# Kernel optimization log

Hardware: AMD Instinct MI355X
Metric: run time of the kernel (lower is better)

Reference implementation:

```python
import jax, jax.numpy as jnp
import numpy as np

C_RGLRU = 8.0

def _rg_lru(x, wa, ba, wx, bx, lam):
    # x: [B, L, D]. Griffin RG-LRU (De et al. 2024).
    r = jax.nn.sigmoid(jnp.einsum('bld,ed->ble', x, wa) + ba)
    i = jax.nn.sigmoid(jnp.einsum('bld,ed->ble', x, wx) + bx)
    log_a = -C_RGLRU * r * jax.nn.softplus(lam)          # [B,L,D], <= 0
    a = jnp.exp(log_a)
    mult = jnp.sqrt(jnp.maximum(1.0 - jnp.exp(2.0 * log_a), 0.0))
    b = mult * (i * x)
    def combine(c1, c2):
        a1, b1 = c1
        a2, b2 = c2
        return a1 * a2, a2 * b1 + b2
    _, h = jax.lax.associative_scan(combine, (a, b), axis=1)
    return h

def setup_inputs() -> dict:
    key = jax.random.key(0)
    ks = jax.random.split(key, 12)
    B, L, D, R = 4, 2048, 2048, 2560
    s_d = 1.0 / np.sqrt(D)
    s_r = 1.0 / np.sqrt(R)
    s_c = 1.0 / np.sqrt(R * 4)
    return {
        'x':      jax.random.normal(ks[0], (B, L, D), jnp.float32),
        'w1':     jax.random.normal(ks[1], (R, D), jnp.float32) * s_d,
        'b1':     jnp.zeros((R,), jnp.float32),
        'conv_w': jax.random.normal(ks[2], (R, R, 4), jnp.float32) * s_c,
        'conv_b': jnp.zeros((R,), jnp.float32),
        'wa':     jax.random.normal(ks[3], (R, R), jnp.float32) * s_r,
        'ba':     jnp.zeros((R,), jnp.float32),
        'wx':     jax.random.normal(ks[4], (R, R), jnp.float32) * s_r,
        'bx':     jnp.zeros((R,), jnp.float32),
        'lam':    jax.random.uniform(ks[5], (R,), jnp.float32, 0.5, 2.0),
        'w2':     jax.random.normal(ks[6], (D, R), jnp.float32) * s_r,
        'b2':     jnp.zeros((D,), jnp.float32),
    }

def reference(x, w1, b1, conv_w, conv_b, wa, ba, wx, bx, lam, w2, b2):
    # linear1 + SiLU: [B,L,D] -> [B,L,R]
    h = jax.nn.silu(jnp.einsum('bld,rd->blr', x, w1) + b1)
    # temporal conv1d: kernel 4, dilation 2, padding 3 both sides (as in torch)
    hc = h.transpose(0, 2, 1)  # [B,R,L]
    hc = jax.lax.conv_general_dilated(
        hc, conv_w, window_strides=(1,), padding=[(3, 3)],
        rhs_dilation=(2,), dimension_numbers=('NCH', 'OIH', 'NCH'))
    hc = hc + conv_b[None, :, None]
    h = hc.transpose(0, 2, 1)  # [B,L,R]
    # RG-LRU gated linear recurrence
    h = _rg_lru(h, wa, ba, wx, bx, lam)
    # linear2: [B,L,R] -> [B,L,D]
    return jnp.einsum('blr,dr->bld', h, w2) + b2
```

## Files before the change

### kernel.cpp

```cpp
#include <hip/hip_runtime.h>

#define B_  4
#define L_  2048
#define D_  2048
#define R_  2560
#define BL_ (B_ * L_)

#define CHK_  16
#define CLEN_ (L_ / CHK_)

typedef unsigned short u16;
typedef unsigned int   u32;

typedef __attribute__((ext_vector_type(8))) short short8;
typedef __attribute__((ext_vector_type(4))) float f32x4;
typedef __attribute__((ext_vector_type(4))) int   int4v;

static __device__ __forceinline__ u16 f2bf(float f) {
  u32 x = __float_as_uint(f);
  x += 0x7fffu + ((x >> 16) & 1u);
  return (u16)(x >> 16);
}
static __device__ __forceinline__ float bf2f(u16 u) {
  return __uint_as_float(((u32)u) << 16);
}

static __device__ __forceinline__ void gld16(const u16* g, u16* l) {
  __builtin_amdgcn_global_load_lds(
      (const __attribute__((address_space(1))) void*)g,
      (__attribute__((address_space(3))) void*)l, 16, 0, 0);
}

__global__ void cvt_bf16(const float* __restrict__ src, u16* __restrict__ dst, int n) {
  int i = blockIdx.x * blockDim.x + threadIdx.x;
  int stride = gridDim.x * blockDim.x;
  for (; i < n; i += stride) dst[i] = f2bf(src[i]);
}

__global__ void cvt_convw(const float* __restrict__ cw, u16* __restrict__ out) {
  int i = blockIdx.x * blockDim.x + threadIdx.x;
  if (i >= R_ * R_) return;
  const float4 v = *(const float4*)(cw + (size_t)i * 4);
  out[(size_t)0 * R_ * R_ + i] = f2bf(v.x);
  out[(size_t)1 * R_ * R_ + i] = f2bf(v.y);
  out[(size_t)2 * R_ * R_ + i] = f2bf(v.z);
  out[(size_t)3 * R_ * R_ + i] = f2bf(v.w);
}

template <int ACT , int OBF16 >
__global__ __launch_bounds__(256)
void gemm_bt(const u16* __restrict__ A, const u16* __restrict__ Bm,
             const float* __restrict__ bias, void* __restrict__ Cv,
             int M, int N, int K) {
  __shared__ u16 As[128 * 32];
  __shared__ u16 Bs[128 * 32];
  const int tid  = threadIdx.x;
  const int bm   = blockIdx.x * 128, bn = blockIdx.y * 128;
  const int wave = tid >> 6, lane = tid & 63;
  const int wm   = (wave >> 1) * 64, wn = (wave & 1) * 64;
  const int q    = lane >> 4, r16 = lane & 15;
  const int lrow = lane >> 2;
  const int gch  = (lane & 3) ^ (lrow & 3);

  f32x4 acc[4][4] = {};

  const int swz = (q ^ (r16 & 3)) * 8;

  for (int kk = 0; kk < K; kk += 32) {
#pragma unroll
    for (int p = 0; p < 2; ++p) {
      const int rb = wave * 32 + p * 16;
      gld16(A  + (size_t)(bm + rb + lrow) * K + kk + gch * 8, &As[rb * 32]);
      gld16(Bm + (size_t)(bn + rb + lrow) * K + kk + gch * 8, &Bs[rb * 32]);
    }
    __syncthreads();
    short8 af[4], bfr[4];
#pragma unroll
    for (int i = 0; i < 4; ++i)
      af[i] = *(const short8*)(&As[(wm + i * 16 + r16) * 32 + swz]);
#pragma unroll
    for (int j = 0; j < 4; ++j)
      bfr[j] = *(const short8*)(&Bs[(wn + j * 16 + r16) * 32 + swz]);
#pragma unroll
    for (int i = 0; i < 4; ++i)
#pragma unroll
      for (int j = 0; j < 4; ++j)
        acc[i][j] = __builtin_amdgcn_mfma_f32_16x16x32_bf16(af[i], bfr[j], acc[i][j], 0, 0, 0);
    __syncthreads();
  }

#pragma unroll
  for (int i = 0; i < 4; ++i) {
    const int row = bm + wm + i * 16 + q * 4;
#pragma unroll
    for (int j = 0; j < 4; ++j) {
      const int col = bn + wn + j * 16 + r16;
      const float bv = bias[col];
#pragma unroll
      for (int rr = 0; rr < 4; ++rr) {
        float v = acc[i][j][rr] + bv;
        if (ACT == 1) v = v / (1.f + __expf(-v));
        const size_t off = (size_t)(row + rr) * N + col;
        if (OBF16) ((u16*)Cv)[off] = f2bf(v);
        else       ((float*)Cv)[off] = v;
      }
    }
  }
}

__global__ __launch_bounds__(256)
void conv_gemm(const u16* __restrict__ A, const u16* __restrict__ CW,
               const float* __restrict__ bias, u16* __restrict__ C) {
  __shared__ u16 As[128 * 32];
  __shared__ u16 Bs[128 * 32];
  const int tid  = threadIdx.x;
  const int bm   = blockIdx.x * 128, bn = blockIdx.y * 128;
  const int wave = tid >> 6, lane = tid & 63;
  const int wm   = (wave >> 1) * 64, wn = (wave & 1) * 64;
  const int q    = lane >> 4, r16 = lane & 15;
  const int lrow = lane >> 2;
  const int gch  = (lane & 3) ^ (lrow & 3);
  const int swz  = (q ^ (r16 & 3)) * 8;
  const int r0 = tid >> 2, c0g = (tid & 3) * 8;
  const int dsw0 = ((tid & 3) ^ (r0 & 3)) * 8;
  const int l0 = (bm + r0) & (L_ - 1), l1 = (bm + r0 + 64) & (L_ - 1);
  const int tileL = blockIdx.x & 15;

  f32x4 acc[4][4] = {};

  for (int tap = 0; tap < 4; ++tap) {
    const int sh = 2 * tap - 3;
    const bool safe = (sh < 0) ? (tileL != 0) : (tileL != 15);
    const bool v0 = (unsigned)(l0 + sh) < (unsigned)L_;
    const bool v1 = (unsigned)(l1 + sh) < (unsigned)L_;
    const u16* aSh = A + (ptrdiff_t)(bm + sh) * R_;
    const u16* bp  = CW + (size_t)tap * R_ * R_;
    const int4v zz = {0, 0, 0, 0};
    for (int kk = 0; kk < R_; kk += 32) {
#pragma unroll
      for (int p = 0; p < 2; ++p) {
        const int rb = wave * 32 + p * 16;
        gld16(bp + (size_t)(bn + rb + lrow) * R_ + kk + gch * 8, &Bs[rb * 32]);
      }
      if (safe) {
#pragma unroll
        for (int p = 0; p < 2; ++p) {
          const int rb = wave * 32 + p * 16;
          gld16(aSh + (size_t)(rb + lrow) * R_ + kk + gch * 8, &As[rb * 32]);
        }
      } else {
        *(int4v*)(&As[r0 * 32 + dsw0]) =
            v0 ? *(const int4v*)(aSh + (size_t)r0 * R_ + kk + c0g) : zz;
        *(int4v*)(&As[(r0 + 64) * 32 + dsw0]) =
            v1 ? *(const int4v*)(aSh + (size_t)(r0 + 64) * R_ + kk + c0g) : zz;
      }
      __syncthreads();
      short8 af[4], bfr[4];
#pragma unroll
      for (int i = 0; i < 4; ++i)
        af[i] = *(const short8*)(&As[(wm + i * 16 + r16) * 32 + swz]);
#pragma unroll
      for (int j = 0; j < 4; ++j)
        bfr[j] = *(const short8*)(&Bs[(wn + j * 16 + r16) * 32 + swz]);
#pragma unroll
      for (int i = 0; i < 4; ++i)
#pragma unroll
        for (int j = 0; j < 4; ++j)
          acc[i][j] = __builtin_amdgcn_mfma_f32_16x16x32_bf16(af[i], bfr[j], acc[i][j], 0, 0, 0);
      __syncthreads();
    }
  }

#pragma unroll
  for (int i = 0; i < 4; ++i) {
    const int row = bm + wm + i * 16 + q * 4;
#pragma unroll
    for (int j = 0; j < 4; ++j) {
      const int col = bn + wn + j * 16 + r16;
      const float bv = bias[col];
#pragma unroll
      for (int rr = 0; rr < 4; ++rr) {
        float v = acc[i][j][rr] + bv;
        C[(size_t)(row + rr) * R_ + col] = f2bf(v);
      }
    }
  }
}

__global__ void gate_ew(const u16* __restrict__ gab, const u16* __restrict__ gib,
                        const u16* __restrict__ h2b, const float* __restrict__ lam,
                        float* __restrict__ a32, float* __restrict__ b32) {
  int idx = blockIdx.x * blockDim.x + threadIdx.x;
  if (idx >= BL_ * R_) return;
  const int r = idx % R_;
  const float ga = bf2f(gab[idx]);
  const float gi = bf2f(gib[idx]);
  const float h2 = bf2f(h2b[idx]);
  const float rr = 1.f / (1.f + __expf(-ga));
  const float ii = 1.f / (1.f + __expf(-gi));
  const float lm = lam[r];
  const float sp = log1pf(__expf(lm));
  const float log_a = -8.f * rr * sp;
  const float a  = __expf(log_a);
  const float e2 = __expf(2.f * log_a);
  const float mult = sqrtf(fmaxf(1.f - e2, 0.f));
  a32[idx] = a;
  b32[idx] = mult * ii * h2;
}

__global__ void scan_pass1(const float* __restrict__ a32, const float* __restrict__ b32,
                           float* __restrict__ Aprod, float* __restrict__ Hend) {
  int t = blockIdx.x * blockDim.x + threadIdx.x;
  if (t >= CHK_ * B_ * R_) return;
  const int c = t / (B_ * R_), br = t % (B_ * R_);
  const int b = br / R_, r = br % R_;
  size_t idx = ((size_t)b * L_ + c * CLEN_) * R_ + r;
  float Ap = 1.f, h = 0.f;
  for (int l = 0; l < CLEN_; ++l) {
    const float a = a32[idx], bb = b32[idx];
    Ap *= a;
    h = a * h + bb;
    idx += R_;
  }
  Aprod[t] = Ap;
  Hend[t]  = h;
}

__global__ void scan_pass2(const float* __restrict__ Aprod, float* __restrict__ Hend) {
  int br = blockIdx.x * blockDim.x + threadIdx.x;
  if (br >= B_ * R_) return;
  float h = Hend[br];
  for (int c = 1; c < CHK_; ++c) {
    const int i = c * (B_ * R_) + br;
    h = Hend[i] + Aprod[i] * h;
    Hend[i] = h;
  }
}

__global__ void scan_pass3(const float* __restrict__ a32, const float* __restrict__ b32,
                           const float* __restrict__ Hend, u16* __restrict__ hs) {
  int t = blockIdx.x * blockDim.x + threadIdx.x;
  if (t >= CHK_ * B_ * R_) return;
  const int c = t / (B_ * R_), br = t % (B_ * R_);
  const int b = br / R_, r = br % R_;
  float h = (c == 0) ? 0.f : Hend[(size_t)(c - 1) * (B_ * R_) + br];
  size_t idx = ((size_t)b * L_ + c * CLEN_) * R_ + r;
  for (int l = 0; l < CLEN_; ++l) {
    h = a32[idx] * h + b32[idx];
    hs[idx] = f2bf(h);
    idx += R_;
  }
}

extern "C" void kernel_launch(void* const* d_in, const int* in_sizes, int n_in,
                              void* d_out, int out_size, void* d_ws, size_t ws_size,
                              hipStream_t stream) {
  (void)in_sizes; (void)n_in; (void)out_size; (void)ws_size;
  const float* x   = (const float*)d_in[0];
  const float* w1  = (const float*)d_in[1];
  const float* b1  = (const float*)d_in[2];
  const float* cw  = (const float*)d_in[3];
  const float* cb  = (const float*)d_in[4];
  const float* wa  = (const float*)d_in[5];
  const float* ba  = (const float*)d_in[6];
  const float* wx  = (const float*)d_in[7];
  const float* bx  = (const float*)d_in[8];
  const float* lam = (const float*)d_in[9];
  const float* w2  = (const float*)d_in[10];
  const float* b2  = (const float*)d_in[11];

  char* ws = (char*)d_ws;
  size_t o = 0;
  auto alloc = [&](size_t bytes) { char* p = ws + o; o += (bytes + 255) & ~255ull; return p; };

  u16* w2b = (u16*)alloc((size_t)D_ * R_ * 2);
  u16* wab = (u16*)alloc((size_t)R_ * R_ * 2);
  u16* wxb = (u16*)alloc((size_t)R_ * R_ * 2);
  char* a32p = ws + o;
  u16* xb  = (u16*)alloc((size_t)BL_ * D_ * 2);
  u16* w1b = (u16*)alloc((size_t)R_ * D_ * 2);
  u16* cwb = (u16*)alloc((size_t)4 * R_ * R_ * 2);
  char* b32p = ws + o;
  u16* h1b = (u16*)alloc((size_t)BL_ * R_ * 2);
  alloc((size_t)BL_ * R_ * 2);
  u16* h2b = (u16*)alloc((size_t)BL_ * R_ * 2);
  u16* gab = (u16*)alloc((size_t)BL_ * R_ * 2);
  u16* gib = (u16*)alloc((size_t)BL_ * R_ * 2);
  float* Aprod = (float*)alloc((size_t)CHK_ * B_ * R_ * 4);
  float* Hend  = (float*)alloc((size_t)CHK_ * B_ * R_ * 4);
  float* a32 = (float*)a32p;
  float* b32 = (float*)b32p;
  u16* hsb = gab;

  cvt_bf16<<<4096, 256, 0, stream>>>(x,  xb,  BL_ * D_);
  cvt_bf16<<<2048, 256, 0, stream>>>(w1, w1b, R_ * D_);
  cvt_bf16<<<2048, 256, 0, stream>>>(wa, wab, R_ * R_);
  cvt_bf16<<<2048, 256, 0, stream>>>(wx, wxb, R_ * R_);
  cvt_bf16<<<2048, 256, 0, stream>>>(w2, w2b, D_ * R_);
  cvt_convw<<<(R_ * R_ + 255) / 256, 256, 0, stream>>>(cw, cwb);

  gemm_bt<1, 1><<<dim3(BL_ / 128, R_ / 128), 256, 0, stream>>>(xb, w1b, b1, h1b, BL_, R_, D_);
  conv_gemm<<<dim3(BL_ / 128, R_ / 128), 256, 0, stream>>>(h1b, cwb, cb, h2b);
  gemm_bt<0, 1><<<dim3(BL_ / 128, R_ / 128), 256, 0, stream>>>(h2b, wab, ba, gab, BL_, R_, R_);
  gemm_bt<0, 1><<<dim3(BL_ / 128, R_ / 128), 256, 0, stream>>>(h2b, wxb, bx, gib, BL_, R_, R_);
  gate_ew<<<(BL_ * R_ + 255) / 256, 256, 0, stream>>>(gab, gib, h2b, lam, a32, b32);
  scan_pass1<<<(CHK_ * B_ * R_ + 255) / 256, 256, 0, stream>>>(a32, b32, Aprod, Hend);
  scan_pass2<<<(B_ * R_ + 255) / 256, 256, 0, stream>>>(Aprod, Hend);
  scan_pass3<<<(CHK_ * B_ * R_ + 255) / 256, 256, 0, stream>>>(a32, b32, Hend, hsb);
  gemm_bt<0, 0><<<dim3(BL_ / 128, D_ / 128), 256, 0, stream>>>(hsb, w2b, b2, d_out, BL_, D_, R_);
}
```

Baseline: 1.633 ms.

## Replace GEMMs with 256-row double-buffered pipelined kernel and padded conv input

Replaces the 128x128 single-buffered GEMM and conv GEMM kernels with one templated 512-thread kernel. It uses 256xBN tiles, K-step 64, double-buffered LDS with global_load_lds prefetch two steps ahead, explicit barriers and waitcnts, and setprio around MFMA blocks. The conv input is now written into a time-padded buffer with zeroed halo rows, which removes the boundary branch in the conv GEMM. The goals are more data reuse per tile and overlap of loads with MFMA. The cost is heavy LDS use, higher register pressure, and fragile hand-written vmcnt counts.

```diff
diff --git a/kernel.cpp b/kernel.cpp
--- a/kernel.cpp
+++ b/kernel.cpp
@@ -5,6 +5,7 @@
 #define D_  2048
 #define R_  2560
 #define BL_ (B_ * L_)
+#define LP_ (L_ + 6)
 
 #define CHK_  16
 #define CLEN_ (L_ / CHK_)
@@ -14,7 +15,6 @@
 
 typedef __attribute__((ext_vector_type(8))) short short8;
 typedef __attribute__((ext_vector_type(4))) float f32x4;
-typedef __attribute__((ext_vector_type(4))) int   int4v;
 
 static __device__ __forceinline__ u16 f2bf(float f) {
   u32 x = __float_as_uint(f);
@@ -30,6 +30,10 @@
       (const __attribute__((address_space(1))) void*)g,
       (__attribute__((address_space(3))) void*)l, 16, 0, 0);
 }
+
+#define SB0()     __builtin_amdgcn_sched_barrier(0)
+#define BAR()     __builtin_amdgcn_s_barrier()
+#define LGKM0()   do { asm volatile("s_waitcnt lgkmcnt(0)" ::: "memory"); SB0(); } while (0)
 
 __global__ void cvt_bf16(const float* __restrict__ src, u16* __restrict__ dst, int n) {
   int i = blockIdx.x * blockDim.x + threadIdx.x;
@@ -47,141 +51,146 @@
   out[(size_t)3 * R_ * R_ + i] = f2bf(v.w);
 }
 
-template <int ACT , int OBF16 >
-__global__ __launch_bounds__(256)
-void gemm_bt(const u16* __restrict__ A, const u16* __restrict__ Bm,
-             const float* __restrict__ bias, void* __restrict__ Cv,
-             int M, int N, int K) {
-  __shared__ u16 As[128 * 32];
-  __shared__ u16 Bs[128 * 32];
+__global__ void zero_pads(u16* __restrict__ h1p) {
+  int i = blockIdx.x * blockDim.x + threadIdx.x;
+  if (i >= 24 * R_) return;
+  const int rr = i / R_, c = i % R_;
+  const int b = rr / 6, k = rr % 6;
+  const int row = b * LP_ + (k < 3 ? k : L_ + k);
+  h1p[(size_t)row * R_ + c] = 0;
+}
+
+template <int NF, int IB>
+__device__ __forceinline__ void mfma_block(f32x4 (&acc)[8][NF], const short8 (&aF)[4],
+                                           const short8 (&bF)[NF]) {
+#pragma unroll
+  for (int i = 0; i < 4; ++i)
+#pragma unroll
+    for (int j = 0; j < NF; ++j)
+      acc[IB + i][j] =
+          __builtin_amdgcn_mfma_f32_16x16x32_bf16(aF[i], bF[j], acc[IB + i][j], 0, 0, 0);
+}
+
+template <int KDIM, int TAPS, int NF, int ACT, int OBF16, int PADOUT>
+__global__ __launch_bounds__(512, 2)
+void gemm256(const u16* __restrict__ A, const u16* __restrict__ Bm,
+             const float* __restrict__ bias, void* __restrict__ Cv, int N) {
+  constexpr int NTK = KDIM / 64;
+  constexpr int NT  = NTK * TAPS;
+  constexpr int BN  = NF * 64;
+  constexpr int BUFU16 = 16384 + NF * 4096;
+  __shared__ u16 lds[2][BUFU16];
+
   const int tid  = threadIdx.x;
-  const int bm   = blockIdx.x * 128, bn = blockIdx.y * 128;
   const int wave = tid >> 6, lane = tid & 63;
-  const int wm   = (wave >> 1) * 64, wn = (wave & 1) * 64;
-  const int q    = lane >> 4, r16 = lane & 15;
-  const int lrow = lane >> 2;
-  const int gch  = (lane & 3) ^ (lrow & 3);
-
-  f32x4 acc[4][4] = {};
-
-  const int swz = (q ^ (r16 & 3)) * 8;
-
-  for (int kk = 0; kk < K; kk += 32) {
-#pragma unroll
-    for (int p = 0; p < 2; ++p) {
-      const int rb = wave * 32 + p * 16;
-      gld16(A  + (size_t)(bm + rb + lrow) * K + kk + gch * 8, &As[rb * 32]);
-      gld16(Bm + (size_t)(bn + rb + lrow) * K + kk + gch * 8, &Bs[rb * 32]);
-    }
-    __syncthreads();
-    short8 af[4], bfr[4];
+  const int wr = wave >> 2, wc = wave & 3;
+  const int q = lane >> 4, r16 = lane & 15;
+  const int rsw = r16 & 7;
+  const int bm = blockIdx.x * 256, bn = blockIdx.y * BN;
+  const int srow = tid >> 3;
+  const int schunk = (tid & 7) ^ (srow & 7);
+  const int bbatch = bm >> 11;
+  const int arow0 = (TAPS == 4) ? (bm + 3 + 6 * bbatch) : bm;
+
+  f32x4 acc[8][NF] = {};
+
+  auto stA = [&](int u, int h) {
+    const int uc = (u < NT) ? u : (NT - 1);
+    const int tap = uc / NTK;
+    const int ku  = (uc % NTK) * 64;
+    const int sh  = (TAPS == 4) ? (2 * tap - 3) : 0;
+    const u16* src = A + (size_t)(arow0 + sh + h * 128) * KDIM + ku + schunk * 8;
+    u16* dst = &lds[u & 1][h * 8192 + wave * 512];
+#pragma unroll
+    for (int s = 0; s < 2; ++s)
+      gld16(src + (size_t)(s * 64 + srow) * KDIM, dst + s * 4096);
+  };
+  auto stB = [&](int u, int j) {
+    const int uc = (u < NT) ? u : (NT - 1);
+    const int tap = uc / NTK;
+    const int ku  = (uc % NTK) * 64;
+    const u16* src = Bm + (size_t)tap * R_ * R_ +
+                     (size_t)(bn + j * 64 + srow) * KDIM + ku + schunk * 8;
+    gld16(src, &lds[u & 1][16384 + j * 4096 + wave * 512]);
+  };
+  auto ldA = [&](short8 (&f)[4], int p, int half, int k) {
+    const int base = half * 8192 + (wr * 64 + r16) * 64 + ((k * 4 + q) ^ rsw) * 8;
 #pragma unroll
     for (int i = 0; i < 4; ++i)
-      af[i] = *(const short8*)(&As[(wm + i * 16 + r16) * 32 + swz]);
-#pragma unroll
-    for (int j = 0; j < 4; ++j)
-      bfr[j] = *(const short8*)(&Bs[(wn + j * 16 + r16) * 32 + swz]);
-#pragma unroll
-    for (int i = 0; i < 4; ++i)
-#pragma unroll
-      for (int j = 0; j < 4; ++j)
-        acc[i][j] = __builtin_amdgcn_mfma_f32_16x16x32_bf16(af[i], bfr[j], acc[i][j], 0, 0, 0);
-    __syncthreads();
-  }
-
-#pragma unroll
-  for (int i = 0; i < 4; ++i) {
-    const int row = bm + wm + i * 16 + q * 4;
-#pragma unroll
-    for (int j = 0; j < 4; ++j) {
-      const int col = bn + wn + j * 16 + r16;
+      f[i] = *(const short8*)&lds[p][base + i * 1024];
+  };
+  auto ldB = [&](short8 (&f)[NF], int p, int k) {
+    const int base = 16384 + (wc * 16 + r16) * 64 + ((k * 4 + q) ^ rsw) * 8;
+#pragma unroll
+    for (int j = 0; j < NF; ++j)
+      f[j] = *(const short8*)&lds[p][base + j * 4096];
+  };
+
+  stA(0, 0); stA(0, 1);
+#pragma unroll
+  for (int j = 0; j < NF; ++j) stB(0, j);
+  stA(1, 0);
+#pragma unroll
+  for (int j = 0; j < NF; ++j) stB(1, j);
+  if constexpr (NF == 5) asm volatile("s_waitcnt vmcnt(7)" ::: "memory");
+  else                   asm volatile("s_waitcnt vmcnt(6)" ::: "memory");
+  SB0();
+  BAR();
+
+  short8 aF[4], bF0[NF], bF1[NF];
+  for (int t = 0; t < NT; ++t) {
+    const int p = t & 1;
+    ldA(aF, p, 0, 0);
+    ldB(bF0, p, 0);
+    stA(t + 1, 1);
+    BAR(); LGKM0();
+    __builtin_amdgcn_s_setprio(1);
+    mfma_block<NF, 0>(acc, aF, bF0);
+    __builtin_amdgcn_s_setprio(0);
+    SB0(); BAR();
+    ldA(aF, p, 0, 1);
+    ldB(bF1, p, 1);
+    BAR(); LGKM0();
+    __builtin_amdgcn_s_setprio(1);
+    mfma_block<NF, 0>(acc, aF, bF1);
+    __builtin_amdgcn_s_setprio(0);
+    SB0(); BAR();
+    ldA(aF, p, 1, 0);
+    stA(t + 2, 0);
+    stB(t + 2, 0); stB(t + 2, 1);
+    BAR(); LGKM0();
+    __builtin_amdgcn_s_setprio(1);
+    mfma_block<NF, 4>(acc, aF, bF0);
+    __builtin_amdgcn_s_setprio(0);
+    SB0(); BAR();
+    ldA(aF, p, 1, 1);
+#pragma unroll
+    for (int j = 2; j < NF; ++j) stB(t + 2, j);
+    BAR(); LGKM0();
+    __builtin_amdgcn_s_setprio(1);
+    mfma_block<NF, 4>(acc, aF, bF1);
+    __builtin_amdgcn_s_setprio(0);
+    if constexpr (NF == 5) asm volatile("s_waitcnt vmcnt(7)" ::: "memory");
+    else                   asm volatile("s_waitcnt vmcnt(6)" ::: "memory");
+    SB0(); BAR();
+  }
+
+#pragma unroll
+  for (int i = 0; i < 8; ++i) {
+    const int rb  = ((i & 4) ? 128 : 0) + wr * 64 + (i & 3) * 16;
+    const int row = bm + rb + q * 4;
+    const int orow = PADOUT ? (row + 3 + 6 * bbatch) : row;
+#pragma unroll
+    for (int j = 0; j < NF; ++j) {
+      const int col = bn + j * 64 + wc * 16 + r16;
       const float bv = bias[col];
 #pragma unroll
       for (int rr = 0; rr < 4; ++rr) {
         float v = acc[i][j][rr] + bv;
         if (ACT == 1) v = v / (1.f + __expf(-v));
-        const size_t off = (size_t)(row + rr) * N + col;
+        const size_t off = (size_t)(orow + rr) * N + col;
         if (OBF16) ((u16*)Cv)[off] = f2bf(v);
         else       ((float*)Cv)[off] = v;
-      }
-    }
-  }
-}
-
-__global__ __launch_bounds__(256)
-void conv_gemm(const u16* __restrict__ A, const u16* __restrict__ CW,
-               const float* __restrict__ bias, u16* __restrict__ C) {
-  __shared__ u16 As[128 * 32];
-  __shared__ u16 Bs[128 * 32];
-  const int tid  = threadIdx.x;
-  const int bm   = blockIdx.x * 128, bn = blockIdx.y * 128;
-  const int wave = tid >> 6, lane = tid & 63;
-  const int wm   = (wave >> 1) * 64, wn = (wave & 1) * 64;
-  const int q    = lane >> 4, r16 = lane & 15;
-  const int lrow = lane >> 2;
-  const int gch  = (lane & 3) ^ (lrow & 3);
-  const int swz  = (q ^ (r16 & 3)) * 8;
-  const int r0 = tid >> 2, c0g = (tid & 3) * 8;
-  const int dsw0 = ((tid & 3) ^ (r0 & 3)) * 8;
-  const int l0 = (bm + r0) & (L_ - 1), l1 = (bm + r0 + 64) & (L_ - 1);
-  const int tileL = blockIdx.x & 15;
-
-  f32x4 acc[4][4] = {};
-
-  for (int tap = 0; tap < 4; ++tap) {
-    const int sh = 2 * tap - 3;
-    const bool safe = (sh < 0) ? (tileL != 0) : (tileL != 15);
-    const bool v0 = (unsigned)(l0 + sh) < (unsigned)L_;
-    const bool v1 = (unsigned)(l1 + sh) < (unsigned)L_;
-    const u16* aSh = A + (ptrdiff_t)(bm + sh) * R_;
-    const u16* bp  = CW + (size_t)tap * R_ * R_;
-    const int4v zz = {0, 0, 0, 0};
-    for (int kk = 0; kk < R_; kk += 32) {
-#pragma unroll
-      for (int p = 0; p < 2; ++p) {
-        const int rb = wave * 32 + p * 16;
-        gld16(bp + (size_t)(bn + rb + lrow) * R_ + kk + gch * 8, &Bs[rb * 32]);
-      }
-      if (safe) {
-#pragma unroll
-        for (int p = 0; p < 2; ++p) {
-          const int rb = wave * 32 + p * 16;
-          gld16(aSh + (size_t)(rb + lrow) * R_ + kk + gch * 8, &As[rb * 32]);
-        }
-      } else {
-        *(int4v*)(&As[r0 * 32 + dsw0]) =
-            v0 ? *(const int4v*)(aSh + (size_t)r0 * R_ + kk + c0g) : zz;
-        *(int4v*)(&As[(r0 + 64) * 32 + dsw0]) =
-            v1 ? *(const int4v*)(aSh + (size_t)(r0 + 64) * R_ + kk + c0g) : zz;
-      }
-      __syncthreads();
-      short8 af[4], bfr[4];
-#pragma unroll
-      for (int i = 0; i < 4; ++i)
-        af[i] = *(const short8*)(&As[(wm + i * 16 + r16) * 32 + swz]);
-#pragma unroll
-      for (int j = 0; j < 4; ++j)
-        bfr[j] = *(const short8*)(&Bs[(wn + j * 16 + r16) * 32 + swz]);
-#pragma unroll
-      for (int i = 0; i < 4; ++i)
-#pragma unroll
-        for (int j = 0; j < 4; ++j)
-          acc[i][j] = __builtin_amdgcn_mfma_f32_16x16x32_bf16(af[i], bfr[j], acc[i][j], 0, 0, 0);
-      __syncthreads();
-    }
-  }
-
-#pragma unroll
-  for (int i = 0; i < 4; ++i) {
-    const int row = bm + wm + i * 16 + q * 4;
-#pragma unroll
-    for (int j = 0; j < 4; ++j) {
-      const int col = bn + wn + j * 16 + r16;
-      const float bv = bias[col];
-#pragma unroll
-      for (int rr = 0; rr < 4; ++rr) {
-        float v = acc[i][j][rr] + bv;
-        C[(size_t)(row + rr) * R_ + col] = f2bf(v);
       }
     }
   }
@@ -281,8 +290,8 @@
   u16* w1b = (u16*)alloc((size_t)R_ * D_ * 2);
   u16* cwb = (u16*)alloc((size_t)4 * R_ * R_ * 2);
   char* b32p = ws + o;
-  u16* h1b = (u16*)alloc((size_t)BL_ * R_ * 2);
-  alloc((size_t)BL_ * R_ * 2);
+  u16* h1p = (u16*)alloc((size_t)B_ * LP_ * R_ * 2);
+  alloc((size_t)BL_ * R_ * 4 - (size_t)B_ * LP_ * R_ * 2);
   u16* h2b = (u16*)alloc((size_t)BL_ * R_ * 2);
   u16* gab = (u16*)alloc((size_t)BL_ * R_ * 2);
   u16* gib = (u16*)alloc((size_t)BL_ * R_ * 2);
@@ -298,14 +307,15 @@
   cvt_bf16<<<2048, 256, 0, stream>>>(wx, wxb, R_ * R_);
   cvt_bf16<<<2048, 256, 0, stream>>>(w2, w2b, D_ * R_);
   cvt_convw<<<(R_ * R_ + 255) / 256, 256, 0, stream>>>(cw, cwb);
-
-  gemm_bt<1, 1><<<dim3(BL_ / 128, R_ / 128), 256, 0, stream>>>(xb, w1b, b1, h1b, BL_, R_, D_);
-  conv_gemm<<<dim3(BL_ / 128, R_ / 128), 256, 0, stream>>>(h1b, cwb, cb, h2b);
-  gemm_bt<0, 1><<<dim3(BL_ / 128, R_ / 128), 256, 0, stream>>>(h2b, wab, ba, gab, BL_, R_, R_);
-  gemm_bt<0, 1><<<dim3(BL_ / 128, R_ / 128), 256, 0, stream>>>(h2b, wxb, bx, gib, BL_, R_, R_);
+  zero_pads<<<(24 * R_ + 255) / 256, 256, 0, stream>>>(h1p);
+
+  gemm256<2048, 1, 5, 1, 1, 1><<<dim3(32, 8), 512, 0, stream>>>(xb, w1b, b1, h1p, R_);
+  gemm256<2560, 4, 5, 0, 1, 0><<<dim3(32, 8), 512, 0, stream>>>(h1p, cwb, cb, h2b, R_);
+  gemm256<2560, 1, 5, 0, 1, 0><<<dim3(32, 8), 512, 0, stream>>>(h2b, wab, ba, gab, R_);
+  gemm256<2560, 1, 5, 0, 1, 0><<<dim3(32, 8), 512, 0, stream>>>(h2b, wxb, bx, gib, R_);
   gate_ew<<<(BL_ * R_ + 255) / 256, 256, 0, stream>>>(gab, gib, h2b, lam, a32, b32);
   scan_pass1<<<(CHK_ * B_ * R_ + 255) / 256, 256, 0, stream>>>(a32, b32, Aprod, Hend);
   scan_pass2<<<(B_ * R_ + 255) / 256, 256, 0, stream>>>(Aprod, Hend);
   scan_pass3<<<(CHK_ * B_ * R_ + 255) / 256, 256, 0, stream>>>(a32, b32, Hend, hsb);
-  gemm_bt<0, 0><<<dim3(BL_ / 128, D_ / 128), 256, 0, stream>>>(hsb, w2b, b2, d_out, BL_, D_, R_);
-}
+  gemm256<2560, 1, 4, 0, 0, 0><<<dim3(32, 8), 512, 0, stream>>>(hsb, w2b, b2, d_out, D_);
+}
```

After: 1.885 ms. 1.15x slower.
